# Optimization experiments

Hardware: AMD Instinct MI355X
Metric: run time of the kernel (lower is better)

Reference implementation:

```python
import jax, jax.numpy as jnp
import numpy as np

VOCAB = 32000
ROUTE_BIAS = 10.0  # weight on the deterministic one-hot route vs mu logits


def setup_inputs() -> dict:
    key = jax.random.key(0)
    k1, k2, k3, k4, k5, k6 = jax.random.split(key, 6)
    B, S, H = 2, 4096, 1024
    E, Ie = 8, 512  # intermediate_size=4096 -> expert_intermediate=512, fused dim=2*Ie=1024
    return {
        "hidden_states": jax.random.normal(k1, (B, S, H), dtype=jnp.float32),
        "token_ids": jax.random.randint(k2, (B, S), 0, VOCAB),
        "mu": jax.random.normal(k3, (B, S, H), dtype=jnp.float32),
        "gate_up_proj": jax.random.normal(k4, (E, H, 2 * Ie), dtype=jnp.float32) * 0.02,
        "down_proj": jax.random.normal(k5, (E, Ie, H), dtype=jnp.float32) * 0.02,
        "mu_router_w": jax.random.normal(k6, (E, H), dtype=jnp.float32) * 0.02,
    }


def reference(hidden_states, token_ids, mu, gate_up_proj, down_proj, mu_router_w):
    B, S, H = hidden_states.shape
    E, _, F2 = gate_up_proj.shape
    Ie = F2 // 2
    N = B * S

    # deterministic token->expert routing, optionally perturbed by mu logits
    token_to_expert = jnp.arange(VOCAB, dtype=jnp.int32) % E
    base_expert = token_to_expert[jnp.clip(token_ids, 0, VOCAB - 1)]      # [B,S]
    mu_logits = jnp.einsum('bsh,eh->bse', mu, mu_router_w)                 # [B,S,E]
    combined = jax.nn.one_hot(base_expert, E, dtype=mu_logits.dtype) * ROUTE_BIAS + mu_logits
    expert_ids = jnp.argmax(combined, axis=-1).reshape(N)                  # [N]

    x = hidden_states.reshape(N, H)
    tok = jnp.arange(N)

    # compute per-expert GEMM then select per-token expert output
    # (same math as gathering the full weight slab per token, without the
    #  N*H*2Ie gathered-weight blowup of the original torch code)
    gu_all = jnp.einsum('nh,ehf->enf', x, gate_up_proj)                    # [E,N,2Ie]
    gu = gu_all[expert_ids, tok]                                           # [N,2Ie]
    gate, up = gu[:, :Ie], gu[:, Ie:]
    inter = jax.nn.silu(gate) * up                                         # [N,Ie]

    z_all = jnp.einsum('ni,eih->enh', inter, down_proj)                    # [E,N,H]
    out = z_all[expert_ids, tok].reshape(B, S, H)
    return out
```

## Files before the change

### kernel.cpp

```cpp
#include <hip/hip_runtime.h>
#include <hip/hip_bf16.h>
#include <stdint.h>

typedef __bf16 bf16x8 __attribute__((ext_vector_type(8)));
typedef float f32x4 __attribute__((ext_vector_type(4)));

#define ROUTE_BIAS_F 10.0f
#define VOCAB_SZ 32000

__device__ __forceinline__ unsigned short f2bf(float f) {
    union { float f; unsigned u; } v; v.f = f;
    unsigned u = v.u;
    unsigned r = u + 0x7FFFu + ((u >> 16) & 1u);
    return (unsigned short)(r >> 16);
}
__device__ __forceinline__ float bf2f(unsigned short s) {
    union { unsigned u; float f; } v; v.u = ((unsigned)s) << 16;
    return v.f;
}
__device__ __forceinline__ void ld16(const unsigned short* g, unsigned short* l) {
    __builtin_amdgcn_global_load_lds(
        (const __attribute__((address_space(1))) void*)g,
        (__attribute__((address_space(3))) void*)l, 16, 0, 0);
}

__global__ void k_prep(const float* __restrict__ hidden, const float* __restrict__ mu,
                       const int* __restrict__ tok_ids, const float* __restrict__ rw,
                       unsigned short* __restrict__ xb, int* __restrict__ eids,
                       int H, int N) {
    int lane = threadIdx.x & 63;
    int wv   = threadIdx.x >> 6;
    int tok  = blockIdx.x * 4 + wv;
    if (tok >= N) return;
    const float4* hp = (const float4*)(hidden + (size_t)tok * H);
    const float4* mp = (const float4*)(mu + (size_t)tok * H);
    const float4* rp = (const float4*)rw;
    ushort4* xp = (ushort4*)(xb + (size_t)tok * H);
    int H4 = H >> 2;
    float acc[8];
#pragma unroll
    for (int e = 0; e < 8; ++e) acc[e] = 0.f;
#pragma unroll
    for (int j = 0; j < 4; ++j) {
        int idx = lane + 64 * j;
        float4 h4 = hp[idx];
        ushort4 o;
        o.x = f2bf(h4.x); o.y = f2bf(h4.y); o.z = f2bf(h4.z); o.w = f2bf(h4.w);
        xp[idx] = o;
        float4 m4 = mp[idx];
#pragma unroll
        for (int e = 0; e < 8; ++e) {
            float4 w4 = rp[e * H4 + idx];
            acc[e] += m4.x * w4.x + m4.y * w4.y + m4.z * w4.z + m4.w * w4.w;
        }
    }
#pragma unroll
    for (int e = 0; e < 8; ++e) {
        float v = acc[e];
#pragma unroll
        for (int off = 32; off > 0; off >>= 1) v += __shfl_xor(v, off);
        acc[e] = v;
    }
    if (lane == 0) {
        int t = tok_ids[tok];
        if (t < 0) t = 0;
        if (t > VOCAB_SZ - 1) t = VOCAB_SZ - 1;
        int be = t % 8;
        float best = -1e30f; int bi = 0;
#pragma unroll
        for (int e = 0; e < 8; ++e) {
            float v = acc[e] + (e == be ? ROUTE_BIAS_F : 0.f);
            if (v > best) { best = v; bi = e; }
        }
        eids[tok] = bi;
    }
}

__global__ __launch_bounds__(256) void k_transpose_all(
        const float* __restrict__ gup, const float* __restrict__ dnp,
        unsigned short* __restrict__ wgut, unsigned short* __restrict__ wdnt,
        int H, int F2, int Ie) {
    __shared__ float tile[64][65];
    int z = blockIdx.z;
    const float* inp; unsigned short* outp; int R, C;
    if (z < 8) { R = H; C = F2; inp = gup + (size_t)z * R * C;       outp = wgut + (size_t)z * R * C; }
    else       { R = Ie; C = H; inp = dnp + (size_t)(z - 8) * R * C; outp = wdnt + (size_t)(z - 8) * R * C; }
    int c0 = blockIdx.x * 64, r0 = blockIdx.y * 64;
    if (r0 >= R) return;
    int tid = threadIdx.x;
    int tr = tid >> 4;
    int tc = (tid & 15) * 4;
#pragma unroll
    for (int p = 0; p < 4; ++p) {
        float4 v = *(const float4*)&inp[(size_t)(r0 + tr + 16 * p) * C + c0 + tc];
        tile[tr + 16 * p][tc + 0] = v.x;
        tile[tr + 16 * p][tc + 1] = v.y;
        tile[tr + 16 * p][tc + 2] = v.z;
        tile[tr + 16 * p][tc + 3] = v.w;
    }
    __syncthreads();
#pragma unroll
    for (int p = 0; p < 4; ++p) {
        int c = tr + 16 * p;
        ushort4 o;
        o.x = f2bf(tile[tc + 0][c]);
        o.y = f2bf(tile[tc + 1][c]);
        o.z = f2bf(tile[tc + 2][c]);
        o.w = f2bf(tile[tc + 3][c]);
        *(ushort4*)&outp[(size_t)(c0 + c) * R + r0 + tc] = o;
    }
}

__global__ void k_count(const int* __restrict__ eids,
                        int* __restrict__ blockcnt, int N) {
    __shared__ int cnt[8];
    int tid = threadIdx.x;
    if (tid < 8) cnt[tid] = 0;
    __syncthreads();
    int tok = blockIdx.x * 256 + tid;
    int lane = tid & 63;
    int eid = (tok < N) ? eids[tok] : -1;
#pragma unroll
    for (int e = 0; e < 8; ++e) {
        unsigned long long m = __ballot(eid == e);
        if (lane == 0 && m) atomicAdd(&cnt[e], __popcll(m));
    }
    __syncthreads();
    if (tid < 8) blockcnt[blockIdx.x * 8 + tid] = cnt[tid];
}

__global__ void k_scan(const int* __restrict__ blockcnt,
                       int* __restrict__ counts, int* __restrict__ base_,
                       int* __restrict__ offs, int NB) {
    __shared__ int tot[8];
    int lane = threadIdx.x;
    int e = lane >> 3, g = lane & 7;
    int v[4];
    int s = 0;
#pragma unroll
    for (int i = 0; i < 4; ++i) { v[i] = s; s += blockcnt[(g * 4 + i) * 8 + e]; }
    int inc = s;
#pragma unroll
    for (int d = 1; d < 8; d <<= 1) {
        int t = __shfl_up(inc, d);
        if (g >= d) inc += t;
    }
    int excl = inc - s;
#pragma unroll
    for (int i = 0; i < 4; ++i) offs[(g * 4 + i) * 8 + e] = excl + v[i];
    if (g == 7) { counts[e] = inc; tot[e] = inc; }
    __syncthreads();
    if (lane == 0) {
        int s2 = 0;
#pragma unroll
        for (int i = 0; i < 8; ++i) { base_[i] = s2; s2 += tot[i]; }
    }
}

__global__ void k_scatter(const int* __restrict__ eids,
                          const int* __restrict__ offs,
                          int* __restrict__ list, int N) {
    __shared__ int wavecnt[4][8];
    int tid = threadIdx.x;
    int lane = tid & 63, wv = tid >> 6;
    int tok = blockIdx.x * 256 + tid;
    int eid = (tok < N) ? eids[tok] : -1;
    unsigned long long below = (1ull << lane) - 1ull;
    int myrank = 0;
#pragma unroll
    for (int e = 0; e < 8; ++e) {
        unsigned long long m = __ballot(eid == e);
        if (lane == 0) wavecnt[wv][e] = __popcll(m);
        if (eid == e) myrank = __popcll(m & below);
    }
    __syncthreads();
    if (eid >= 0) {
        int pre = 0;
        for (int w = 0; w < wv; ++w) pre += wavecnt[w][eid];
        int pos = offs[blockIdx.x * 8 + eid] + pre + myrank;
        list[eid * N + pos] = tok;
    }
}

#define TM 128
#define TN 128
#define TK 64

__global__ __launch_bounds__(256, 3) void k_gemm_gateup(
    const unsigned short* __restrict__ X,
    const unsigned short* __restrict__ Wt,
    unsigned short* __restrict__ IT,
    const int* __restrict__ counts, const int* __restrict__ base_,
    const int* __restrict__ list, int N, int H, int Ie) {
    int bid = blockIdx.x;
    int e = bid & 7;
    int t = bid >> 3;
    int nt = t & 7;
    int mt = t >> 3;
    int cnt = counts[e];
    int m0 = mt * TM;
    if (m0 >= cnt) return;
    int F2 = 2 * Ie;

    __shared__ __align__(16) unsigned short As[TM * TK];
    __shared__ __align__(16) unsigned short Bs[TN * TK];

    int tid = threadIdx.x;
    int lane = tid & 63, wv = tid >> 6;
    int wr = (wv >> 1) * 64;
    int wc = (wv & 1) * 64;

    int rowg = lane >> 3;
    int sl   = (lane & 7) ^ rowg;

    const unsigned short* ag[4];
    const unsigned short* bg[4];
#pragma unroll
    for (int i = 0; i < 4; ++i) {
        int r = wv * 32 + i * 8 + rowg;
        int gr = m0 + r;
        int tokrow = (gr < cnt) ? list[e * N + gr] : 0;
        ag[i] = X + (size_t)tokrow * H + sl * 8;
    }
#pragma unroll
    for (int i = 0; i < 4; ++i) {
        int r = wv * 32 + i * 8 + rowg;
        int wrow = (r & 1) * Ie + nt * 64 + (r >> 1);
        bg[i] = Wt + ((size_t)e * F2 + wrow) * H + sl * 8;
    }

    f32x4 acc[4][4];
#pragma unroll
    for (int i = 0; i < 4; ++i)
#pragma unroll
        for (int j = 0; j < 4; ++j) acc[i][j] = (f32x4)(0.f);

    int q = lane >> 4, m = lane & 15;
    int sw = m & 7;

    for (int k0 = 0; k0 < H; k0 += TK) {
#pragma unroll
        for (int i = 0; i < 4; ++i)
            ld16(ag[i] + k0, &As[(wv * 32 + i * 8) * TK]);
#pragma unroll
        for (int i = 0; i < 4; ++i)
            ld16(bg[i] + k0, &Bs[(wv * 32 + i * 8) * TK]);
        __syncthreads();
#pragma unroll
        for (int ks = 0; ks < TK; ks += 32) {
            int kc = ks >> 3;
            int ck = ((kc + q) ^ sw) << 3;
            bf16x8 af[4], bfr[4];
#pragma unroll
            for (int im = 0; im < 4; ++im)
                af[im] = *(const bf16x8*)&As[(wr + m + im * 16) * TK + ck];
#pragma unroll
            for (int in_ = 0; in_ < 4; ++in_)
                bfr[in_] = *(const bf16x8*)&Bs[(wc + m + in_ * 16) * TK + ck];
#pragma unroll
            for (int im = 0; im < 4; ++im)
#pragma unroll
                for (int in_ = 0; in_ < 4; ++in_)
                    acc[im][in_] = __builtin_amdgcn_mfma_f32_16x16x32_bf16(
                        af[im], bfr[in_], acc[im][in_], 0, 0, 0);
        }
        __syncthreads();
    }

    int b = base_[e];
    int nt64 = nt * 64;
#pragma unroll
    for (int im = 0; im < 4; ++im) {
#pragma unroll
        for (int j = 0; j < 4; ++j) {
            int row = wr + im * 16 + q * 4 + j;
            int gr = m0 + row;
#pragma unroll
            for (int in_ = 0; in_ < 4; ++in_) {
                float v = acc[im][in_][j];
                float u = __shfl_xor(v, 1);
                float g = v;
                float s = g / (1.f + __expf(-g));
                float res = s * u;
                if (!(lane & 1) && gr < cnt) {
                    int oc = nt64 + ((wc + in_ * 16 + m) >> 1);
                    IT[(size_t)(b + gr) * Ie + oc] = f2bf(res);
                }
            }
        }
    }
}

__global__ __launch_bounds__(256, 3) void k_gemm_down(
    const unsigned short* __restrict__ IT,
    const unsigned short* __restrict__ Wt,
    float* __restrict__ OUT,
    const int* __restrict__ counts, const int* __restrict__ base_,
    const int* __restrict__ list, int N, int Ie, int H) {
    int bid = blockIdx.x;
    int e = bid & 7;
    int t = bid >> 3;
    int nt = t & 7;
    int mt = t >> 3;
    int cnt = counts[e];
    int m0 = mt * TM;
    if (m0 >= cnt) return;
    int n0 = nt * TN;
    int b = base_[e];

    __shared__ __align__(16) unsigned short As[TM * TK];
    __shared__ __align__(16) unsigned short Bs[TN * TK];

    int tid = threadIdx.x;
    int lane = tid & 63, wv = tid >> 6;
    int wr = (wv >> 1) * 64;
    int wc = (wv & 1) * 64;

    int rowg = lane >> 3;
    int sl   = (lane & 7) ^ rowg;

    const unsigned short* We = Wt + ((size_t)e * H + n0) * Ie;
    const unsigned short* ag[4];
    const unsigned short* bg[4];
#pragma unroll
    for (int i = 0; i < 4; ++i) {
        int r = wv * 32 + i * 8 + rowg;
        int gr = m0 + r;
        int arow = (gr < cnt) ? (b + gr) : b;
        ag[i] = IT + (size_t)arow * Ie + sl * 8;
    }
#pragma unroll
    for (int i = 0; i < 4; ++i) {
        int r = wv * 32 + i * 8 + rowg;
        bg[i] = We + (size_t)r * Ie + sl * 8;
    }

    f32x4 acc[4][4];
#pragma unroll
    for (int i = 0; i < 4; ++i)
#pragma unroll
        for (int j = 0; j < 4; ++j) acc[i][j] = (f32x4)(0.f);

    int q = lane >> 4, m = lane & 15;
    int sw = m & 7;

    for (int k0 = 0; k0 < Ie; k0 += TK) {
#pragma unroll
        for (int i = 0; i < 4; ++i)
            ld16(ag[i] + k0, &As[(wv * 32 + i * 8) * TK]);
#pragma unroll
        for (int i = 0; i < 4; ++i)
            ld16(bg[i] + k0, &Bs[(wv * 32 + i * 8) * TK]);
        __syncthreads();
#pragma unroll
        for (int ks = 0; ks < TK; ks += 32) {
            int kc = ks >> 3;
            int ck = ((kc + q) ^ sw) << 3;
            bf16x8 af[4], bfr[4];
#pragma unroll
            for (int im = 0; im < 4; ++im)
                af[im] = *(const bf16x8*)&As[(wr + m + im * 16) * TK + ck];
#pragma unroll
            for (int in_ = 0; in_ < 4; ++in_)
                bfr[in_] = *(const bf16x8*)&Bs[(wc + m + in_ * 16) * TK + ck];
#pragma unroll
            for (int im = 0; im < 4; ++im)
#pragma unroll
                for (int in_ = 0; in_ < 4; ++in_)
                    acc[im][in_] = __builtin_amdgcn_mfma_f32_16x16x32_bf16(
                        af[im], bfr[in_], acc[im][in_], 0, 0, 0);
        }
        __syncthreads();
    }

#pragma unroll
    for (int im = 0; im < 4; ++im) {
#pragma unroll
        for (int j = 0; j < 4; ++j) {
            int row = wr + im * 16 + q * 4 + j;
            int gr = m0 + row;
            if (gr < cnt) {
                int tok = list[e * N + gr];
                float* orow = OUT + (size_t)tok * H + n0;
#pragma unroll
                for (int in_ = 0; in_ < 4; ++in_) {
                    int col = wc + in_ * 16 + m;
                    orow[col] = acc[im][in_][j];
                }
            }
        }
    }
}

extern "C" void kernel_launch(void* const* d_in, const int* in_sizes, int n_in,
                              void* d_out, int out_size, void* d_ws, size_t ws_size,
                              hipStream_t stream) {
    const float* hidden   = (const float*)d_in[0];
    const int*   tok_ids  = (const int*)d_in[1];
    const float* mu       = (const float*)d_in[2];
    const float* gup      = (const float*)d_in[3];
    const float* dnp      = (const float*)d_in[4];
    const float* rw       = (const float*)d_in[5];
    float* out = (float*)d_out;

    int N  = in_sizes[1];
    int H  = in_sizes[0] / N;
    int E  = in_sizes[5] / H;
    int F2 = in_sizes[3] / (E * H);
    int Ie = F2 / 2;

    int NB = (N + 255) / 256;

    char* ws = (char*)d_ws;
    size_t o = 0;
    auto alloc = [&](size_t sz) {
        size_t r = o;
        o += (sz + 255) & ~(size_t)255;
        return r;
    };
    int* counts   = (int*)(ws + alloc((size_t)E * 4));
    int* base_    = (int*)(ws + alloc((size_t)E * 4));
    int* eids     = (int*)(ws + alloc((size_t)N * 4));
    int* blockcnt = (int*)(ws + alloc((size_t)NB * 8 * 4));
    int* offs     = (int*)(ws + alloc((size_t)NB * 8 * 4));
    int* list     = (int*)(ws + alloc((size_t)E * N * 4));
    unsigned short* xb   = (unsigned short*)(ws + alloc((size_t)N * H * 2));
    unsigned short* wgut = (unsigned short*)(ws + alloc((size_t)E * F2 * H * 2));
    unsigned short* wdnt = (unsigned short*)(ws + alloc((size_t)E * H * Ie * 2));
    unsigned short* it   = (unsigned short*)(ws + alloc((size_t)N * Ie * 2));

    k_prep<<<dim3((N + 3) / 4), dim3(256), 0, stream>>>(hidden, mu, tok_ids, rw, xb, eids, H, N);

    k_transpose_all<<<dim3(16, 16, 16), dim3(256), 0, stream>>>(gup, dnp, wgut, wdnt, H, F2, Ie);

    k_count<<<dim3(NB), dim3(256), 0, stream>>>(eids, blockcnt, N);
    k_scan<<<dim3(1), dim3(64), 0, stream>>>(blockcnt, counts, base_, offs, NB);
    k_scatter<<<dim3(NB), dim3(256), 0, stream>>>(eids, offs, list, N);

    int MT = (N + TM - 1) / TM;
    k_gemm_gateup<<<dim3(E * MT * (Ie / 64)), dim3(256), 0, stream>>>(
        xb, wgut, it, counts, base_, list, N, H, Ie);

    k_gemm_down<<<dim3(E * MT * (H / TN)), dim3(256), 0, stream>>>(
        it, wdnt, out, counts, base_, list, N, Ie, H);
}
```

Baseline: 219.0 us.

## Double-buffer LDS tiles in both expert GEMM kernels to overlap loads with MFMA

Both grouped GEMM kernels now hold two LDS buffers for the A and B tiles. The next K-tile is issued via global_load_lds into the alternate buffer while MFMAs run on the current one, which removes one barrier per iteration and is meant to hide global load latency. LDS per block doubles to 64KB and launch bounds drop from 3 to 2 blocks per CU, so occupancy falls. The single remaining barrier per iteration relies on the hardware waiting for outstanding LDS-direct loads before __syncthreads.

```diff
diff --git a/kernel.cpp b/kernel.cpp
--- a/kernel.cpp
+++ b/kernel.cpp
@@ -186,7 +186,7 @@
 #define TN 128
 #define TK 64
 
-__global__ __launch_bounds__(256, 3) void k_gemm_gateup(
+__global__ __launch_bounds__(256, 2) void k_gemm_gateup(
     const unsigned short* __restrict__ X,
     const unsigned short* __restrict__ Wt,
     unsigned short* __restrict__ IT,
@@ -202,8 +202,8 @@
     if (m0 >= cnt) return;
     int F2 = 2 * Ie;
 
-    __shared__ __align__(16) unsigned short As[TM * TK];
-    __shared__ __align__(16) unsigned short Bs[TN * TK];
+    __shared__ __align__(16) unsigned short As[2][TM * TK];
+    __shared__ __align__(16) unsigned short Bs[2][TN * TK];
 
     int tid = threadIdx.x;
     int lane = tid & 63, wv = tid >> 6;
@@ -238,14 +238,24 @@
     int q = lane >> 4, m = lane & 15;
     int sw = m & 7;
 
-    for (int k0 = 0; k0 < H; k0 += TK) {
-#pragma unroll
-        for (int i = 0; i < 4; ++i)
-            ld16(ag[i] + k0, &As[(wv * 32 + i * 8) * TK]);
-#pragma unroll
-        for (int i = 0; i < 4; ++i)
-            ld16(bg[i] + k0, &Bs[(wv * 32 + i * 8) * TK]);
-        __syncthreads();
+    int nk = H / TK;
+#pragma unroll
+    for (int i = 0; i < 4; ++i) ld16(ag[i], &As[0][(wv * 32 + i * 8) * TK]);
+#pragma unroll
+    for (int i = 0; i < 4; ++i) ld16(bg[i], &Bs[0][(wv * 32 + i * 8) * TK]);
+    __syncthreads();
+
+    int cur = 0;
+    for (int t_ = 0; t_ < nk; ++t_) {
+        if (t_ + 1 < nk) {
+            int k1 = (t_ + 1) * TK;
+#pragma unroll
+            for (int i = 0; i < 4; ++i) ld16(ag[i] + k1, &As[cur ^ 1][(wv * 32 + i * 8) * TK]);
+#pragma unroll
+            for (int i = 0; i < 4; ++i) ld16(bg[i] + k1, &Bs[cur ^ 1][(wv * 32 + i * 8) * TK]);
+        }
+        const unsigned short* Ac = As[cur];
+        const unsigned short* Bc = Bs[cur];
 #pragma unroll
         for (int ks = 0; ks < TK; ks += 32) {
             int kc = ks >> 3;
@@ -253,10 +263,10 @@
             bf16x8 af[4], bfr[4];
 #pragma unroll
             for (int im = 0; im < 4; ++im)
-                af[im] = *(const bf16x8*)&As[(wr + m + im * 16) * TK + ck];
+                af[im] = *(const bf16x8*)&Ac[(wr + m + im * 16) * TK + ck];
 #pragma unroll
             for (int in_ = 0; in_ < 4; ++in_)
-                bfr[in_] = *(const bf16x8*)&Bs[(wc + m + in_ * 16) * TK + ck];
+                bfr[in_] = *(const bf16x8*)&Bc[(wc + m + in_ * 16) * TK + ck];
 #pragma unroll
             for (int im = 0; im < 4; ++im)
 #pragma unroll
@@ -265,6 +275,7 @@
                         af[im], bfr[in_], acc[im][in_], 0, 0, 0);
         }
         __syncthreads();
+        cur ^= 1;
     }
 
     int b = base_[e];
@@ -291,7 +302,7 @@
     }
 }
 
-__global__ __launch_bounds__(256, 3) void k_gemm_down(
+__global__ __launch_bounds__(256, 2) void k_gemm_down(
     const unsigned short* __restrict__ IT,
     const unsigned short* __restrict__ Wt,
     float* __restrict__ OUT,
@@ -308,8 +319,8 @@
     int n0 = nt * TN;
     int b = base_[e];
 
-    __shared__ __align__(16) unsigned short As[TM * TK];
-    __shared__ __align__(16) unsigned short Bs[TN * TK];
+    __shared__ __align__(16) unsigned short As[2][TM * TK];
+    __shared__ __align__(16) unsigned short Bs[2][TN * TK];
 
     int tid = threadIdx.x;
     int lane = tid & 63, wv = tid >> 6;
@@ -344,14 +355,24 @@
     int q = lane >> 4, m = lane & 15;
     int sw = m & 7;
 
-    for (int k0 = 0; k0 < Ie; k0 += TK) {
-#pragma unroll
-        for (int i = 0; i < 4; ++i)
-            ld16(ag[i] + k0, &As[(wv * 32 + i * 8) * TK]);
-#pragma unroll
-        for (int i = 0; i < 4; ++i)
-            ld16(bg[i] + k0, &Bs[(wv * 32 + i * 8) * TK]);
-        __syncthreads();
+    int nk = Ie / TK;
+#pragma unroll
+    for (int i = 0; i < 4; ++i) ld16(ag[i], &As[0][(wv * 32 + i * 8) * TK]);
+#pragma unroll
+    for (int i = 0; i < 4; ++i) ld16(bg[i], &Bs[0][(wv * 32 + i * 8) * TK]);
+    __syncthreads();
+
+    int cur = 0;
+    for (int t_ = 0; t_ < nk; ++t_) {
+        if (t_ + 1 < nk) {
+            int k1 = (t_ + 1) * TK;
+#pragma unroll
+            for (int i = 0; i < 4; ++i) ld16(ag[i] + k1, &As[cur ^ 1][(wv * 32 + i * 8) * TK]);
+#pragma unroll
+            for (int i = 0; i < 4; ++i) ld16(bg[i] + k1, &Bs[cur ^ 1][(wv * 32 + i * 8) * TK]);
+        }
+        const unsigned short* Ac = As[cur];
+        const unsigned short* Bc = Bs[cur];
 #pragma unroll
         for (int ks = 0; ks < TK; ks += 32) {
             int kc = ks >> 3;
@@ -359,10 +380,10 @@
             bf16x8 af[4], bfr[4];
 #pragma unroll
             for (int im = 0; im < 4; ++im)
-                af[im] = *(const bf16x8*)&As[(wr + m + im * 16) * TK + ck];
+                af[im] = *(const bf16x8*)&Ac[(wr + m + im * 16) * TK + ck];
 #pragma unroll
             for (int in_ = 0; in_ < 4; ++in_)
-                bfr[in_] = *(const bf16x8*)&Bs[(wc + m + in_ * 16) * TK + ck];
+                bfr[in_] = *(const bf16x8*)&Bc[(wc + m + in_ * 16) * TK + ck];
 #pragma unroll
             for (int im = 0; im < 4; ++im)
 #pragma unroll
@@ -371,6 +392,7 @@
                         af[im], bfr[in_], acc[im][in_], 0, 0, 0);
         }
         __syncthreads();
+        cur ^= 1;
     }
 
 #pragma unroll
```

Result: slower. 239.4 us (+9.3%).
